# Kernel tuning notes

Measured on AMD Instinct MI355X. Metric: run time of the kernel, lower is better.

## Reference

```python
import jax, jax.numpy as jnp
import numpy as np

# Grouped TF->gene sparse decoder dims
T = 512       # number of TFs (tf_size)
K = 4         # nodes_per_tf (width_multiplier); decoder_features = T*K = 2048
G = 20000     # number of genes (gene_size)
EPG = 3       # regulating TFs per gene (TF-gene edges per gene)
B = 512       # batch of cells


def setup_inputs() -> dict:
    key = jax.random.key(0)
    k0, k1, k2, k3, k4, k5, k6 = jax.random.split(key, 7)
    features = jax.random.normal(k0, (B, T), dtype=jnp.float32)
    # Layer 1: each TF fans out to its own K hidden nodes (one weight per edge)
    w1 = jax.random.normal(k1, (T, K), dtype=jnp.float32) * 0.5
    b1 = jax.random.normal(k2, (T, K), dtype=jnp.float32) * 0.1
    # Layer 2: block-dense KxK mixing within each TF group
    w2 = jax.random.normal(k3, (T, K, K), dtype=jnp.float32) * (1.0 / np.sqrt(K))
    b2 = jax.random.normal(k4, (T, K), dtype=jnp.float32) * 0.1
    # Output layer: gene g sums over its EPG TF edges x K hidden nodes
    w3 = jax.random.normal(k5, (G, EPG, K), dtype=jnp.float32) * (1.0 / np.sqrt(EPG * K))
    b3 = jax.random.normal(k6, (G,), dtype=jnp.float32) * 0.1
    # Fixed irregular TF-gene connectivity (constant structure, like data_obj)
    edge_tf = jnp.asarray(
        np.random.default_rng(0).integers(0, T, size=(G, EPG)), dtype=jnp.int32
    )
    return {"features": features, "w1": w1, "b1": b1, "w2": w2, "b2": b2,
            "w3": w3, "b3": b3, "edge_tf": edge_tf}


def reference(features, w1, b1, w2, b2, w3, b3, edge_tf):
    # SparseLinear decoder_1: TF t -> its K hidden nodes, then LeakyReLU(0.01)
    h1 = jax.nn.leaky_relu(features[:, :, None] * w1 + b1)            # [B,T,K]
    # SparseLinear decoder_2: block-dense within each TF group + LeakyReLU
    h2 = jax.nn.leaky_relu(jnp.einsum('btj,tjk->btk', h1, w2) + b2)   # [B,T,K]
    # SparseLinear output: gather each gene's regulating TF groups, contract
    gathered = h2[:, edge_tf, :]                                      # [B,G,EPG,K]
    out = jnp.einsum('bgek,gek->bg', gathered, w3) + b3               # [B,G]
    return out
```

## Files before the change

kernel.cpp:

```cpp
#include <hip/hip_runtime.h>

namespace {

constexpr int T = 512;
constexpr int K = 4;
constexpr int G = 20000;
constexpr int EPG = 3;
constexpr int B = 512;
constexpr int BT = 4;
constexpr int NSLAB = B / BT;
constexpr int NG = 8;
constexpr int GPB = 2560;
constexpr int NCHUNK = GPB / 256;
constexpr int RS = 20;
constexpr float SLOPE = 0.01f;

__device__ __forceinline__ float lrelu(float x) { return fmaxf(x, SLOPE * x); }
__device__ __forceinline__ float dot4(float4 a, float4 b) {
  return a.x * b.x + a.y * b.y + a.z * b.z + a.w * b.w;
}

__global__ __launch_bounds__(256, 4) void fused_kernel(
    const float* __restrict__ features, const float* __restrict__ w1,
    const float* __restrict__ b1, const float* __restrict__ w2,
    const float* __restrict__ b2, const float* __restrict__ w3,
    const float* __restrict__ b3, const int* __restrict__ edge,
    float* __restrict__ out) {
  __shared__ float lds[T * RS];
  const int tid = threadIdx.x;
  const int b0 = blockIdx.x * BT;
  const int gbase = blockIdx.y * GPB;

#pragma unroll
  for (int half = 0; half < 2; ++half) {
    const int t = half * 256 + tid;
    const float4 W1 = reinterpret_cast<const float4*>(w1)[t];
    const float4 B1 = reinterpret_cast<const float4*>(b1)[t];
    const float4 B2 = reinterpret_cast<const float4*>(b2)[t];
    const float4* W2 = reinterpret_cast<const float4*>(w2) + t * 4;
    const float4 r0 = W2[0];
    const float4 r1 = W2[1];
    const float4 r2 = W2[2];
    const float4 r3 = W2[3];
#pragma unroll
    for (int b = 0; b < BT; ++b) {
      const float f = features[(size_t)(b0 + b) * T + t];
      const float h0 = lrelu(f * W1.x + B1.x);
      const float h1 = lrelu(f * W1.y + B1.y);
      const float h2 = lrelu(f * W1.z + B1.z);
      const float h3 = lrelu(f * W1.w + B1.w);
      float4 o;
      o.x = lrelu(B2.x + h0 * r0.x + h1 * r1.x + h2 * r2.x + h3 * r3.x);
      o.y = lrelu(B2.y + h0 * r0.y + h1 * r1.y + h2 * r2.y + h3 * r3.y);
      o.z = lrelu(B2.z + h0 * r0.z + h1 * r1.z + h2 * r2.z + h3 * r3.z);
      o.w = lrelu(B2.w + h0 * r0.w + h1 * r1.w + h2 * r2.w + h3 * r3.w);
      *reinterpret_cast<float4*>(&lds[t * RS + b * 4]) = o;
    }
  }
  __syncthreads();

  const char* ldsc = reinterpret_cast<const char*>(lds);

  float4 pw0, pw1, pw2;
  int po0, po1, po2;
  float pb;
  auto load_chunk = [&](int s) {
    const int g = gbase + s * 256 + tid;
    if (g < G) {
      const float4* wp = reinterpret_cast<const float4*>(w3 + (size_t)g * (EPG * K));
      pw0 = wp[0];
      pw1 = wp[1];
      pw2 = wp[2];
      po0 = edge[g * EPG + 0] * (RS * 4);
      po1 = edge[g * EPG + 1] * (RS * 4);
      po2 = edge[g * EPG + 2] * (RS * 4);
      pb = b3[g];
    } else {
      pw0 = pw1 = pw2 = make_float4(0.f, 0.f, 0.f, 0.f);
      po0 = po1 = po2 = 0;
      pb = 0.f;
    }
  };
  load_chunk(0);

  for (int s = 0; s < NCHUNK; ++s) {
    const float4 c0 = pw0, c1 = pw1, c2 = pw2;
    const int o0 = po0, o1 = po1, o2 = po2;
    const float bias = pb;
    const int g = gbase + s * 256 + tid;
    if (s + 1 < NCHUNK) load_chunk(s + 1);

    float a0 = bias, a1 = bias, a2 = bias, a3 = bias;
    {
      const float4 v0 = *reinterpret_cast<const float4*>(ldsc + o0);
      const float4 v1 = *reinterpret_cast<const float4*>(ldsc + o0 + 16);
      const float4 v2 = *reinterpret_cast<const float4*>(ldsc + o0 + 32);
      const float4 v3 = *reinterpret_cast<const float4*>(ldsc + o0 + 48);
      a0 += dot4(v0, c0); a1 += dot4(v1, c0); a2 += dot4(v2, c0); a3 += dot4(v3, c0);
    }
    {
      const float4 v0 = *reinterpret_cast<const float4*>(ldsc + o1);
      const float4 v1 = *reinterpret_cast<const float4*>(ldsc + o1 + 16);
      const float4 v2 = *reinterpret_cast<const float4*>(ldsc + o1 + 32);
      const float4 v3 = *reinterpret_cast<const float4*>(ldsc + o1 + 48);
      a0 += dot4(v0, c1); a1 += dot4(v1, c1); a2 += dot4(v2, c1); a3 += dot4(v3, c1);
    }
    {
      const float4 v0 = *reinterpret_cast<const float4*>(ldsc + o2);
      const float4 v1 = *reinterpret_cast<const float4*>(ldsc + o2 + 16);
      const float4 v2 = *reinterpret_cast<const float4*>(ldsc + o2 + 32);
      const float4 v3 = *reinterpret_cast<const float4*>(ldsc + o2 + 48);
      a0 += dot4(v0, c2); a1 += dot4(v1, c2); a2 += dot4(v2, c2); a3 += dot4(v3, c2);
    }
    if (g < G) {
      out[(size_t)(b0 + 0) * G + g] = a0;
      out[(size_t)(b0 + 1) * G + g] = a1;
      out[(size_t)(b0 + 2) * G + g] = a2;
      out[(size_t)(b0 + 3) * G + g] = a3;
    }
  }
}

}

extern "C" void kernel_launch(void* const* d_in, const int* in_sizes, int n_in,
                              void* d_out, int out_size, void* d_ws, size_t ws_size,
                              hipStream_t stream) {
  const float* features = (const float*)d_in[0];
  const float* w1 = (const float*)d_in[1];
  const float* b1 = (const float*)d_in[2];
  const float* w2 = (const float*)d_in[3];
  const float* b2 = (const float*)d_in[4];
  const float* w3 = (const float*)d_in[5];
  const float* b3 = (const float*)d_in[6];
  const int* edge = (const int*)d_in[7];
  float* out = (float*)d_out;

  dim3 grid(NSLAB, NG);
  fused_kernel<<<grid, 256, 0, stream>>>(features, w1, b1, w2, b2, w3, b3, edge,
                                         out);
}
```

Before: 92.52 us.

## Pre-pack gene weights, bias and edge offsets into SoA float4 arrays; nontemporal output stores

Adds a prep kernel that reorganises w3, b3 and edge indices into four structure-of-arrays float4 buffers in the workspace, padded to the grid size. The main kernel then reads them with fully coalesced 16-byte loads and no bounds checks, replacing the strided 48-byte AoS weight loads and scattered int loads. Output writes become nontemporal stores to avoid polluting cache with the large output. The prep kernel runs every call, so it adds a launch and one extra pass over roughly 1.3 MB of data.

```diff
diff --git a/kernel.cpp b/kernel.cpp
--- a/kernel.cpp
+++ b/kernel.cpp
@@ -12,6 +12,7 @@
 constexpr int NG = 8;
 constexpr int GPB = 2560;
 constexpr int NCHUNK = GPB / 256;
+constexpr int GPAD = NG * GPB;
 constexpr int RS = 20;
 constexpr float SLOPE = 0.01f;
 
@@ -20,12 +21,33 @@
   return a.x * b.x + a.y * b.y + a.z * b.z + a.w * b.w;
 }
 
+__global__ __launch_bounds__(256) void prep_kernel(
+    const float* __restrict__ w3, const float* __restrict__ b3,
+    const int* __restrict__ edge, float4* __restrict__ R0,
+    float4* __restrict__ R1, float4* __restrict__ R2, float4* __restrict__ RM) {
+  const int g = blockIdx.x * 256 + threadIdx.x;
+  float4 a = make_float4(0.f, 0.f, 0.f, 0.f), b = a, c = a, m = a;
+  if (g < G) {
+    const float4* wp = reinterpret_cast<const float4*>(w3 + (size_t)g * (EPG * K));
+    a = wp[0];
+    b = wp[1];
+    c = wp[2];
+    m.x = b3[g];
+    m.y = __int_as_float(edge[g * EPG + 0] * (RS * 4));
+    m.z = __int_as_float(edge[g * EPG + 1] * (RS * 4));
+    m.w = __int_as_float(edge[g * EPG + 2] * (RS * 4));
+  } else {
+    m.y = m.z = m.w = __int_as_float(0);
+  }
+  R0[g] = a; R1[g] = b; R2[g] = c; RM[g] = m;
+}
+
 __global__ __launch_bounds__(256, 4) void fused_kernel(
     const float* __restrict__ features, const float* __restrict__ w1,
     const float* __restrict__ b1, const float* __restrict__ w2,
-    const float* __restrict__ b2, const float* __restrict__ w3,
-    const float* __restrict__ b3, const int* __restrict__ edge,
-    float* __restrict__ out) {
+    const float* __restrict__ b2, const float4* __restrict__ R0,
+    const float4* __restrict__ R1, const float4* __restrict__ R2,
+    const float4* __restrict__ RM, float* __restrict__ out) {
   __shared__ float lds[T * RS];
   const int tid = threadIdx.x;
   const int b0 = blockIdx.x * BT;
@@ -61,36 +83,22 @@
 
   const char* ldsc = reinterpret_cast<const char*>(lds);
 
-  float4 pw0, pw1, pw2;
-  int po0, po1, po2;
-  float pb;
-  auto load_chunk = [&](int s) {
-    const int g = gbase + s * 256 + tid;
-    if (g < G) {
-      const float4* wp = reinterpret_cast<const float4*>(w3 + (size_t)g * (EPG * K));
-      pw0 = wp[0];
-      pw1 = wp[1];
-      pw2 = wp[2];
-      po0 = edge[g * EPG + 0] * (RS * 4);
-      po1 = edge[g * EPG + 1] * (RS * 4);
-      po2 = edge[g * EPG + 2] * (RS * 4);
-      pb = b3[g];
-    } else {
-      pw0 = pw1 = pw2 = make_float4(0.f, 0.f, 0.f, 0.f);
-      po0 = po1 = po2 = 0;
-      pb = 0.f;
-    }
-  };
-  load_chunk(0);
+  float4 pw0 = R0[gbase + tid];
+  float4 pw1 = R1[gbase + tid];
+  float4 pw2 = R2[gbase + tid];
+  float4 pm = RM[gbase + tid];
 
   for (int s = 0; s < NCHUNK; ++s) {
-    const float4 c0 = pw0, c1 = pw1, c2 = pw2;
-    const int o0 = po0, o1 = po1, o2 = po2;
-    const float bias = pb;
+    const float4 c0 = pw0, c1 = pw1, c2 = pw2, cm = pm;
     const int g = gbase + s * 256 + tid;
-    if (s + 1 < NCHUNK) load_chunk(s + 1);
-
-    float a0 = bias, a1 = bias, a2 = bias, a3 = bias;
+    if (s + 1 < NCHUNK) {
+      const int gn = gbase + (s + 1) * 256 + tid;
+      pw0 = R0[gn]; pw1 = R1[gn]; pw2 = R2[gn]; pm = RM[gn];
+    }
+    const int o0 = __float_as_int(cm.y);
+    const int o1 = __float_as_int(cm.z);
+    const int o2 = __float_as_int(cm.w);
+    float a0 = cm.x, a1 = cm.x, a2 = cm.x, a3 = cm.x;
     {
       const float4 v0 = *reinterpret_cast<const float4*>(ldsc + o0);
       const float4 v1 = *reinterpret_cast<const float4*>(ldsc + o0 + 16);
@@ -113,10 +121,10 @@
       a0 += dot4(v0, c2); a1 += dot4(v1, c2); a2 += dot4(v2, c2); a3 += dot4(v3, c2);
     }
     if (g < G) {
-      out[(size_t)(b0 + 0) * G + g] = a0;
-      out[(size_t)(b0 + 1) * G + g] = a1;
-      out[(size_t)(b0 + 2) * G + g] = a2;
-      out[(size_t)(b0 + 3) * G + g] = a3;
+      __builtin_nontemporal_store(a0, &out[(size_t)(b0 + 0) * G + g]);
+      __builtin_nontemporal_store(a1, &out[(size_t)(b0 + 1) * G + g]);
+      __builtin_nontemporal_store(a2, &out[(size_t)(b0 + 2) * G + g]);
+      __builtin_nontemporal_store(a3, &out[(size_t)(b0 + 3) * G + g]);
     }
   }
 }
@@ -136,7 +144,14 @@
   const int* edge = (const int*)d_in[7];
   float* out = (float*)d_out;
 
+  float4* R0 = (float4*)d_ws;
+  float4* R1 = R0 + GPAD;
+  float4* R2 = R1 + GPAD;
+  float4* RM = R2 + GPAD;
+
+  prep_kernel<<<GPAD / 256, 256, 0, stream>>>(w3, b3, edge, R0, R1, R2, RM);
+
   dim3 grid(NSLAB, NG);
-  fused_kernel<<<grid, 256, 0, stream>>>(features, w1, b1, w2, b2, w3, b3, edge,
-                                         out);
+  fused_kernel<<<grid, 256, 0, stream>>>(features, w1, b1, w2, b2, R0, R1, R2,
+                                         RM, out);
 }
```

Result: no change. 93.67 us (+1.2%).
